# Optimization experiments

Hardware: AMD Instinct MI355X
Metric: run time of the kernel (lower is better)

Reference implementation:

```python
import jax, jax.numpy as jnp
import numpy as np

B, DIM, DIMH, DIMC = 1024, 32, 1024, 512
SQRT_HALF_PI = float(np.sqrt(np.pi / 2.0))
SQRT2 = float(np.sqrt(2.0))


def _gsp(x):
    """gaussian_softplus activation from ConditionalICNN."""
    return (SQRT_HALF_PI * x * jax.scipy.special.erf(x / SQRT2)
            + jnp.exp(-0.5 * x * x) + SQRT_HALF_PI * x) / (2.0 * SQRT_HALF_PI)


def setup_inputs() -> dict:
    key = jax.random.key(0)
    _i = [0]
    def nrm(shape, s=0.05):
        _i[0] += 1
        return jax.random.normal(jax.random.fold_in(key, _i[0]), shape, dtype=jnp.float32) * s
    inp = {
        "x": nrm((B, DIM), 1.0),
        "c": nrm((B, DIMC), 1.0),
        # w0 init: log(exp(1)-1) as in DeepConvexFlow
        "w0": jnp.full((1,), float(np.log(np.e - 1.0)), dtype=jnp.float32),
        "w1": jnp.zeros((1,), dtype=jnp.float32),
        "Wz0_w": nrm((DIMH, DIM)), "Wz0_b": nrm((DIMH,)),
        "Wc0_w": nrm((DIMH, DIMC)), "Wc0_b": nrm((DIMH,)),
        "an0_b": nrm((DIMH,)), "an0_logs": nrm((DIMH,), 0.01),
        "Wz1_w": nrm((DIMH, DIMH)), "Wz1_b": nrm((DIMH,)),
        "Wx1_w": nrm((DIMH, DIM)), "Wx1_b": nrm((DIMH,)),
        "Wc1_w": nrm((DIMH, DIMC)), "Wc1_b": nrm((DIMH,)),
        "an1_b": nrm((DIMH,)), "an1_logs": nrm((DIMH,), 0.01),
        "Wz2_w": nrm((DIMH, DIMH)), "Wz2_b": nrm((DIMH,)),
        "Wx2_w": nrm((DIMH, DIM)), "Wx2_b": nrm((DIMH,)),
        "Wc2_w": nrm((DIMH, DIMC)), "Wc2_b": nrm((DIMH,)),
        "an2_b": nrm((DIMH,)), "an2_logs": nrm((DIMH,), 0.01),
        "Wzout_w": nrm((1, DIMH)), "Wxout_w": nrm((1, DIM)), "Wcout_w": nrm((1, DIMC)),
    }
    return inp


def reference(x, c, w0, w1,
              Wz0_w, Wz0_b, Wc0_w, Wc0_b, an0_b, an0_logs,
              Wz1_w, Wz1_b, Wx1_w, Wx1_b, Wc1_w, Wc1_b, an1_b, an1_logs,
              Wz2_w, Wz2_b, Wx2_w, Wx2_b, Wc2_w, Wc2_b, an2_b, an2_logs,
              Wzout_w, Wxout_w, Wcout_w):
    """ConditionalDeepConvexFlow.forward_transform with exact logdet.
    Returns (f = grad_x F(x), logdet = logabsdet of per-sample Hessian)."""

    def pot(x1, c1):  # scalar convex potential F for one sample
        h = Wz0_w @ x1 + Wz0_b + Wc0_w @ c1 + Wc0_b
        z = _gsp((h + an0_b) * jnp.exp(an0_logs))  # ActNormNoLogdet + act
        for (Wz_w, Wz_b, Wx_w, Wx_b, Wc_w, Wc_b, an_b, an_logs) in (
                (Wz1_w, Wz1_b, Wx1_w, Wx1_b, Wc1_w, Wc1_b, an1_b, an1_logs),
                (Wz2_w, Wz2_b, Wx2_w, Wx2_b, Wc2_w, Wc2_b, an2_b, an2_logs)):
            # PosLinear: softplus(W) with gain 1/in_features
            h = (jax.nn.softplus(Wz_w) @ z) / DIMH + Wz_b \
                + Wx_w @ x1 + Wx_b + Wc_w @ c1 + Wc_b
            z = _gsp((h + an_b) * jnp.exp(an_logs))
        icnn = (jax.nn.softplus(Wzout_w) @ z)[0] / DIMH \
               + (Wxout_w @ x1)[0] + (Wcout_w @ c1)[0]
        return jax.nn.softplus(w1)[0] * icnn \
               + jax.nn.softplus(w0)[0] * 0.5 * jnp.sum(x1 * x1)

    f = jax.vmap(jax.grad(pot))(x, c)          # [B, DIM]
    H = jax.vmap(jax.hessian(pot))(x, c)       # [B, DIM, DIM]
    logdet = jnp.linalg.slogdet(H)[1]          # [B]
    return f, logdet
```

## Files before the change

kernel.cpp:

```cpp
#include <hip/hip_runtime.h>

constexpr int NB   = 1024;
constexpr int NDIM = 32;
constexpr int NH   = 1024;
constexpr int NC   = 512;
constexpr int NS   = 8;
constexpr int KSF  = 8;

constexpr float INV_SQRT2PI = 0.3989422804014327f;
constexpr float SQRT_HALF   = 0.70710678118654752f;
constexpr float SQRT_HPI    = 1.2533141373155003f;

typedef __attribute__((ext_vector_type(8))) short short8;
typedef __attribute__((ext_vector_type(4))) short short4v;
typedef __attribute__((ext_vector_type(4))) float float4v;

__device__ __forceinline__ float sp_f(float x) {
  return (x > 20.f) ? x : log1pf(expf(x));
}

__device__ __forceinline__ short f2bf(float f) {
  union { float f; unsigned u; } x; x.f = f;
  const unsigned r = x.u + 0x7fffu + ((x.u >> 16) & 1u);
  return (short)(r >> 16);
}

__device__ __forceinline__ float bf2f(short s) {
  union { unsigned u; float f; } c;
  c.u = ((unsigned)(unsigned short)s) << 16;
  return c.f;
}

__device__ __forceinline__ void async_ld16(const void* g, void* l) {
  __builtin_amdgcn_global_load_lds(
      (const __attribute__((address_space(1))) void*)g,
      (__attribute__((address_space(3))) void*)l, 16, 0, 0);
}

__global__ __launch_bounds__(256) void k_prep(
    const float* __restrict__ Wz1, const float* __restrict__ Wz2,
    const float* __restrict__ Wzout, const float* __restrict__ Wz0,
    const float* __restrict__ Wx1, const float* __restrict__ Wx2,
    const float* __restrict__ Wc0, const float* __restrict__ Wc1,
    const float* __restrict__ Wc2, const float* __restrict__ Cc,
    short* __restrict__ S1b, short* __restrict__ S1Tb,
    short* __restrict__ S2b, short* __restrict__ S2Tb,
    short* __restrict__ Wc0b, short* __restrict__ Wc1b, short* __restrict__ Wc2b,
    short* __restrict__ Ccb, short* __restrict__ W0Tb,
    short* __restrict__ Wx1Tb, short* __restrict__ Wx2Tb,
    float* __restrict__ so)
{
  const int idx = blockIdx.x * 256 + threadIdx.x;
  const int i = idx >> 10, p = idx & 1023;
  const float v1 = sp_f(Wz1[idx]);
  const short b1 = f2bf(v1);
  S1b[idx] = b1; S1Tb[p * NH + i] = b1;
  const float v2 = sp_f(Wz2[idx]);
  const short b2 = f2bf(v2);
  S2b[idx] = b2; S2Tb[p * NH + i] = b2;
  if (idx < NH) so[idx] = sp_f(Wzout[idx]);
  if (idx < NH * NC) {
    Wc0b[idx] = f2bf(Wc0[idx]);
    Wc1b[idx] = f2bf(Wc1[idx]);
    Wc2b[idx] = f2bf(Wc2[idx]);
  }
  if (idx < NB * NC) Ccb[idx] = f2bf(Cc[idx]);
  if (idx < NDIM * NH) {
    const int j = idx >> 10, pp = idx & 1023;
    W0Tb[idx]  = f2bf(Wz0[pp * NDIM + j]);
    Wx1Tb[idx] = f2bf(Wx1[pp * NDIM + j]);
    Wx2Tb[idx] = f2bf(Wx2[pp * NDIM + j]);
  }
}

__global__ __launch_bounds__(256) void k_gemmx(
    const float* __restrict__ A,
    const float* __restrict__ B0, const float* __restrict__ B1,
    const float* __restrict__ B2,
    float* __restrict__ C0, float* __restrict__ C1, float* __restrict__ C2,
    int ldc)
{
  const float* Bt = (blockIdx.z == 0) ? B0 : (blockIdx.z == 1) ? B1 : B2;
  float* C        = (blockIdx.z == 0) ? C0 : (blockIdx.z == 1) ? C1 : C2;
  __shared__ float As[16][68];
  __shared__ float Bs[16][68];
  const int tid  = threadIdx.y * 16 + threadIdx.x;
  const int arow = tid >> 2;
  const int acol = (tid & 3) << 2;
  const int m0 = blockIdx.y << 6;
  const int n0 = blockIdx.x << 6;

  float acc[4][4];
#pragma unroll
  for (int i = 0; i < 4; ++i)
#pragma unroll
    for (int j = 0; j < 4; ++j) acc[i][j] = 0.f;

  const int R = m0 + arow;
  for (int k0 = 0; k0 < NDIM; k0 += 16) {
    const float4 av = *reinterpret_cast<const float4*>(&A[(size_t)R * NDIM + k0 + acol]);
    As[acol + 0][arow] = av.x; As[acol + 1][arow] = av.y;
    As[acol + 2][arow] = av.z; As[acol + 3][arow] = av.w;
    const float4 bv = *reinterpret_cast<const float4*>(&Bt[(size_t)(n0 + arow) * NDIM + k0 + acol]);
    Bs[acol + 0][arow] = bv.x; Bs[acol + 1][arow] = bv.y;
    Bs[acol + 2][arow] = bv.z; Bs[acol + 3][arow] = bv.w;
    __syncthreads();
#pragma unroll
    for (int kk = 0; kk < 16; ++kk) {
      const float4 a  = *reinterpret_cast<const float4*>(&As[kk][threadIdx.y << 2]);
      const float4 bb = *reinterpret_cast<const float4*>(&Bs[kk][threadIdx.x << 2]);
      const float am[4] = {a.x, a.y, a.z, a.w};
      const float bn[4] = {bb.x, bb.y, bb.z, bb.w};
#pragma unroll
      for (int i2 = 0; i2 < 4; ++i2)
#pragma unroll
        for (int j2 = 0; j2 < 4; ++j2)
          acc[i2][j2] = fmaf(am[i2], bn[j2], acc[i2][j2]);
    }
    __syncthreads();
  }
#pragma unroll
  for (int i2 = 0; i2 < 4; ++i2) {
    const int row = m0 + (threadIdx.y << 2) + i2;
    const int col = n0 + (threadIdx.x << 2);
    float* cp = &C[(size_t)row * ldc + col];
    const float4 cur = *reinterpret_cast<const float4*>(cp);
    float4 o;
    o.x = acc[i2][0] + cur.x; o.y = acc[i2][1] + cur.y;
    o.z = acc[i2][2] + cur.z; o.w = acc[i2][3] + cur.w;
    *reinterpret_cast<float4*>(cp) = o;
  }
}

__global__ __launch_bounds__(256) void k_m128(
    const short* __restrict__ A, const short* __restrict__ Bt,
    float* __restrict__ C, float scale, int K, int ldc)
{
  __shared__ short As[128 * 32];
  __shared__ short Bs[128 * 32];
  const int tid  = threadIdx.x;
  const int wave = tid >> 6, lane = tid & 63;
  const int m0 = blockIdx.x << 7, n0 = blockIdx.y << 7;
  const int wm = (wave >> 1) << 6, wn = (wave & 1) << 6;
  const int qd = lane >> 4, md = lane & 15;
  const int sr = lane >> 2;
  const int sc = (lane & 3) << 3;

  float4v acc[4][4];
#pragma unroll
  for (int i = 0; i < 4; ++i)
#pragma unroll
    for (int j = 0; j < 4; ++j) acc[i][j] = (float4v)(0.f);

  for (int k0 = 0; k0 < K; k0 += 32) {
#pragma unroll
    for (int i = 0; i < 2; ++i) {
      const int ch  = wave * 2 + i;
      const int row = ch * 16 + sr;
      async_ld16(&A [(size_t)(m0 + row) * K + k0 + sc], &As[ch * 512]);
      async_ld16(&Bt[(size_t)(n0 + row) * K + k0 + sc], &Bs[ch * 512]);
    }
    __syncthreads();
    short8 af[4], bfr[4];
#pragma unroll
    for (int t = 0; t < 4; ++t) {
      af[t]  = *(const short8*)&As[(wm + t * 16 + md) * 32 + qd * 8];
      bfr[t] = *(const short8*)&Bs[(wn + t * 16 + md) * 32 + qd * 8];
    }
#pragma unroll
    for (int i = 0; i < 4; ++i)
#pragma unroll
      for (int j = 0; j < 4; ++j)
        acc[i][j] = __builtin_amdgcn_mfma_f32_16x16x32_bf16(bfr[j], af[i], acc[i][j], 0, 0, 0);
    __syncthreads();
  }

#pragma unroll
  for (int i = 0; i < 4; ++i) {
    const int rowg = m0 + wm + i * 16 + md;
#pragma unroll
    for (int j = 0; j < 4; ++j) {
      const int colb = n0 + wn + j * 16 + (qd << 2);
      float4 o;
      o.x = acc[i][j][0] * scale; o.y = acc[i][j][1] * scale;
      o.z = acc[i][j][2] * scale; o.w = acc[i][j][3] * scale;
      *reinterpret_cast<float4*>(&C[(size_t)rowg * ldc + colb]) = o;
    }
  }
}

template<int EPI>
__global__ __launch_bounds__(256) void k_mgemm(
    const short* __restrict__ A, const short* __restrict__ Bt,
    short* __restrict__ o1, short* __restrict__ o2,
    const float* __restrict__ gvec, const float* __restrict__ dvec,
    const short* __restrict__ wepiT,
    float scale, int K, int b0)
{
  __shared__ short As[128 * 32];
  __shared__ short Bs[64 * 32];
  const int tid  = threadIdx.x;
  const int wave = tid >> 6, lane = tid & 63;
  const int m0 = blockIdx.x << 7, n0 = blockIdx.y << 6;
  const int wm = (wave >> 1) << 6, wn = (wave & 1) << 5;
  const int qd = lane >> 4, md = lane & 15;
  const int sr = lane >> 2;
  const int sc = (lane & 3) << 3;

  float4v acc[4][2];
#pragma unroll
  for (int i = 0; i < 4; ++i)
#pragma unroll
    for (int j = 0; j < 2; ++j) acc[i][j] = (float4v)(0.f);

  for (int k0 = 0; k0 < K; k0 += 32) {
#pragma unroll
    for (int i = 0; i < 3; ++i) {
      const int ch = wave * 3 + i;
      if (ch < 8) {
        async_ld16(&A[(size_t)(m0 + ch * 16 + sr) * K + k0 + sc], &As[ch * 512]);
      } else {
        const int c2 = ch - 8;
        async_ld16(&Bt[(size_t)(n0 + c2 * 16 + sr) * K + k0 + sc], &Bs[c2 * 512]);
      }
    }
    __syncthreads();
    short8 af[4], bfr[2];
#pragma unroll
    for (int t = 0; t < 4; ++t)
      af[t]  = *(const short8*)&As[(wm + t * 16 + md) * 32 + qd * 8];
#pragma unroll
    for (int t = 0; t < 2; ++t)
      bfr[t] = *(const short8*)&Bs[(wn + t * 16 + md) * 32 + qd * 8];
#pragma unroll
    for (int i = 0; i < 4; ++i)
#pragma unroll
      for (int j = 0; j < 2; ++j)
        acc[i][j] = __builtin_amdgcn_mfma_f32_16x16x32_bf16(bfr[j], af[i], acc[i][j], 0, 0, 0);
    __syncthreads();
  }

  const int bbase = b0 + ((m0 + wm) >> 5);
  const size_t bNH0 = (size_t)bbase * NH, bNH1 = bNH0 + NH;
  float4 dqA[2], dqB[2], ggA[2], ggB[2];
#pragma unroll
  for (int j = 0; j < 2; ++j) {
    const int colb = n0 + wn + j * 16 + (qd << 2);
    dqA[j] = *(const float4*)&dvec[bNH0 + colb];
    dqB[j] = *(const float4*)&dvec[bNH1 + colb];
    if constexpr (EPI == 2) {
      ggA[j] = *(const float4*)&gvec[bNH0 + colb];
      ggB[j] = *(const float4*)&gvec[bNH1 + colb];
    }
  }
#pragma unroll
  for (int i = 0; i < 4; ++i) {
    const int rowg = m0 + wm + i * 16 + md;
    const int j2 = rowg & 31;
#pragma unroll
    for (int j = 0; j < 2; ++j) {
      const int colb = n0 + wn + j * 16 + (qd << 2);
      const short4v wq = *(const short4v*)&wepiT[(size_t)j2 * NH + colb];
      const float4 dq = (i < 2) ? dqA[j] : dqB[j];
      const float dqv[4] = {dq.x, dq.y, dq.z, dq.w};
      float v[4];
      short4v o1v;
#pragma unroll
      for (int r = 0; r < 4; ++r) {
        v[r] = acc[i][j][r] * scale + bf2f(wq[r]);
        o1v[r] = f2bf(v[r] * dqv[r]);
      }
      *(short4v*)&o1[(size_t)rowg * NH + colb] = o1v;
      if constexpr (EPI == 2) {
        const float4 gg = (i < 2) ? ggA[j] : ggB[j];
        const float ggv[4] = {gg.x, gg.y, gg.z, gg.w};
        short4v o2v;
#pragma unroll
        for (int r = 0; r < 4; ++r) o2v[r] = f2bf(v[r] * ggv[r]);
        *(short4v*)&o2[(size_t)rowg * NH + colb] = o2v;
      }
    }
  }
}

__global__ __launch_bounds__(256) void k_mgemm64(
    const short* __restrict__ A, const short* __restrict__ Bt,
    float* __restrict__ Cpart)
{
  __shared__ short As[64 * 32];
  __shared__ short Bs[64 * 32];
  const int tid  = threadIdx.x;
  const int wave = tid >> 6, lane = tid & 63;
  const int m0 = blockIdx.x << 6, n0 = blockIdx.y << 6;
  const int kb = blockIdx.z << 9;
  const int wm = (wave >> 1) << 5, wn = (wave & 1) << 5;
  const int qd = lane >> 4, md = lane & 15;
  const int sr = lane >> 2;
  const int sc = (lane & 3) << 3;

  float4v acc[2][2];
#pragma unroll
  for (int i = 0; i < 2; ++i)
#pragma unroll
    for (int j = 0; j < 2; ++j) acc[i][j] = (float4v)(0.f);

  for (int k0 = kb; k0 < kb + 512; k0 += 32) {
    const int row = wave * 16 + sr;
    async_ld16(&A [(size_t)(m0 + row) * NH + k0 + sc], &As[wave * 512]);
    async_ld16(&Bt[(size_t)(n0 + row) * NH + k0 + sc], &Bs[wave * 512]);
    __syncthreads();
    short8 af[2], bfr[2];
#pragma unroll
    for (int t = 0; t < 2; ++t) {
      af[t]  = *(const short8*)&As[(wm + t * 16 + md) * 32 + qd * 8];
      bfr[t] = *(const short8*)&Bs[(wn + t * 16 + md) * 32 + qd * 8];
    }
#pragma unroll
    for (int i = 0; i < 2; ++i)
#pragma unroll
      for (int j = 0; j < 2; ++j)
        acc[i][j] = __builtin_amdgcn_mfma_f32_16x16x32_bf16(bfr[j], af[i], acc[i][j], 0, 0, 0);
    __syncthreads();
  }

  float* out = Cpart + (size_t)blockIdx.z * NB * NH;
#pragma unroll
  for (int i = 0; i < 2; ++i) {
    const int rowg = m0 + wm + i * 16 + md;
#pragma unroll
    for (int j = 0; j < 2; ++j) {
      const int colb = n0 + wn + j * 16 + (qd << 2);
      float4 o;
      o.x = acc[i][j][0]; o.y = acc[i][j][1];
      o.z = acc[i][j][2]; o.w = acc[i][j][3];
      *reinterpret_cast<float4*>(&out[(size_t)rowg * NH + colb]) = o;
    }
  }
}

__global__ __launch_bounds__(256) void k_act(
    const float* __restrict__ HP2, const float* __restrict__ HPC_l,
    const float* __restrict__ bA, const float* __restrict__ bB,
    const float* __restrict__ bC,
    const float* __restrict__ anb, const float* __restrict__ anl,
    short* __restrict__ Zbf, float* __restrict__ G, float* __restrict__ U,
    int hasC, float scale)
{
  const int idx = blockIdx.x * 256 + threadIdx.x;
  const int i = idx & 1023;
  float bias = bA[i] + bB[i] + anb[i];
  if (hasC) bias += bC[i];
  const float el = expf(anl[i]);
  const float hc = HPC_l[(size_t)(idx >> 10) * (3 * NH) + i];
  const float hp = HP2 ? (HP2[idx] + HP2[(size_t)NB * NH + idx]) * scale : 0.f;
  const float a = (hp + hc + bias) * el;
  const float pdf = expf(-0.5f * a * a);
  const float er = erff(a * SQRT_HALF);
  Zbf[idx] = f2bf((SQRT_HPI * a * er + pdf + SQRT_HPI * a) * INV_SQRT2PI);
  G[idx] = 0.5f * (1.f + er) * el;
  U[idx] = pdf * INV_SQRT2PI * el * el;
}

__global__ __launch_bounds__(256) void k_act2(
    const float* __restrict__ HP2, const float* __restrict__ HPC_l,
    const float* __restrict__ bA, const float* __restrict__ bB,
    const float* __restrict__ bC,
    const float* __restrict__ anb, const float* __restrict__ anl,
    const float* __restrict__ so,
    float* __restrict__ SD2, short* __restrict__ D2gbf, float scale)
{
  const int idx = blockIdx.x * 256 + threadIdx.x;
  const int i = idx & 1023;
  const float bias = bA[i] + bB[i] + bC[i] + anb[i];
  const float el = expf(anl[i]);
  const float hc = HPC_l[(size_t)(idx >> 10) * (3 * NH) + i];
  const float hp = (HP2[idx] + HP2[(size_t)NB * NH + idx]) * scale;
  const float a = (hp + hc + bias) * el;
  const float pdf = expf(-0.5f * a * a);
  const float er = erff(a * SQRT_HALF);
  const float g = 0.5f * (1.f + er) * el;
  const float u = pdf * INV_SQRT2PI * el * el;
  const float t2 = so[i] * (1.f / NH);
  SD2[idx] = sqrtf(fmaxf(t2 * u, 0.f));
  D2gbf[idx] = f2bf(t2 * g);
}

__global__ __launch_bounds__(256) void k_bw1(
    const float* __restrict__ T2, const float* __restrict__ G1,
    const float* __restrict__ U1,
    short* __restrict__ E1bf, float* __restrict__ SD1, float scale)
{
  const int idx = blockIdx.x * 256 + threadIdx.x;
  const float t = (T2[idx] + T2[(size_t)NB * NH + idx]) * scale;
  E1bf[idx] = f2bf(t * G1[idx]);
  SD1[idx] = sqrtf(fmaxf(t * U1[idx], 0.f));
}

__global__ __launch_bounds__(256) void k_bw0(
    const float* __restrict__ T2, const float* __restrict__ U0,
    const float* __restrict__ G0,
    float* __restrict__ D0, short* __restrict__ GT0b, float scale)
{
  const int idx = blockIdx.x * 256 + threadIdx.x;
  const float t = (T2[idx] + T2[(size_t)NB * NH + idx]) * scale;
  D0[idx] = t * U0[idx];
  GT0b[idx] = f2bf(t * G0[idx]);
}

__global__ __launch_bounds__(256) void k_scale0(
    const float* __restrict__ G0, const float* __restrict__ Wz0,
    short* __restrict__ Ah1, int b0)
{
  const int idx = blockIdx.x * 256 + threadIdx.x;
  const int p = idx & 1023, r = idx >> 10;
  const int b = b0 + (r >> 5), j = r & 31;
  Ah1[idx] = f2bf(G0[(size_t)b * NH + p] * Wz0[p * NDIM + j]);
}

__global__ __launch_bounds__(256) void k_fgemm(
    const short* __restrict__ A0, const short* __restrict__ A1,
    const short* __restrict__ A2,
    const short* __restrict__ W0T, const short* __restrict__ W1T,
    const short* __restrict__ W2T,
    float* __restrict__ partF)
{
  const int mb = blockIdx.x;
  const int ks = blockIdx.y;
  const int term = blockIdx.z;
  const short* A  = (term == 0) ? A0 : (term == 1) ? A1 : A2;
  const short* WT = (term == 0) ? W0T : (term == 1) ? W1T : W2T;
  const int wave = threadIdx.x >> 6, lane = threadIdx.x & 63;
  const int qd = lane >> 4, md = lane & 15;
  const int m0 = mb * 128 + wave * 32;
  const int kbeg = ks * (NH / KSF);

  float4v acc[2][2];
#pragma unroll
  for (int i = 0; i < 2; ++i)
#pragma unroll
    for (int j = 0; j < 2; ++j) acc[i][j] = (float4v)(0.f);

  for (int k0 = kbeg; k0 < kbeg + NH / KSF; k0 += 32) {
    const int kk = k0 + qd * 8;
    short8 af[2], bfr[2];
    af[0]  = *(const short8*)&A[(size_t)(m0 + md) * NH + kk];
    af[1]  = *(const short8*)&A[(size_t)(m0 + 16 + md) * NH + kk];
    bfr[0] = *(const short8*)&WT[(size_t)md * NH + kk];
    bfr[1] = *(const short8*)&WT[(size_t)(16 + md) * NH + kk];
#pragma unroll
    for (int i = 0; i < 2; ++i)
#pragma unroll
      for (int j = 0; j < 2; ++j)
        acc[i][j] = __builtin_amdgcn_mfma_f32_16x16x32_bf16(af[i], bfr[j], acc[i][j], 0, 0, 0);
  }

  float* out = &partF[(size_t)(term * KSF + ks) * NB * 32];
#pragma unroll
  for (int i = 0; i < 2; ++i)
#pragma unroll
    for (int j = 0; j < 2; ++j)
#pragma unroll
      for (int r = 0; r < 4; ++r) {
        const int row = m0 + i * 16 + qd * 4 + r;
        const int col = j * 16 + md;
        out[(size_t)row * 32 + col] = acc[i][j][r];
      }
}

__global__ __launch_bounds__(256) void k_fred(
    const float* __restrict__ partF, const float* __restrict__ X,
    const float* __restrict__ Wxout,
    const float* __restrict__ w0p, const float* __restrict__ w1p,
    float* __restrict__ outF)
{
  const int e = blockIdx.x * 256 + threadIdx.x;
  float s = 0.f;
#pragma unroll
  for (int p = 0; p < 3 * KSF; ++p) s += partF[(size_t)p * NB * 32 + e];
  const float spw0 = sp_f(w0p[0]);
  const float spw1 = sp_f(w1p[0]);
  outF[e] = spw1 * (s + Wxout[e & 31]) + spw0 * X[e];
}

__global__ __launch_bounds__(256) void k_gram(
    const short* __restrict__ Q1, const short* __restrict__ Q2,
    const short* __restrict__ W0T, const float* __restrict__ D0,
    float* __restrict__ partH, int b0)
{
  const int ns = blockIdx.x, bl = blockIdx.y;
  const int b = b0 + bl;
  const int wave = threadIdx.x >> 6, lane = threadIdx.x & 63;
  const int wm = (wave >> 1) << 4, wn = (wave & 1) << 4;
  const int qd = lane >> 4, md = lane & 15;
  const int kbeg = ns << 7;
  const size_t rb = (size_t)bl * 32 * NH;

  float4v acc = (float4v)(0.f);

  for (int k0 = kbeg; k0 < kbeg + 128; k0 += 32) {
    const int kk = k0 + qd * 8;
    const short8 ar = *(const short8*)&W0T[(size_t)(wm + md) * NH + kk];
    float dd[8];
    *(float4*)&dd[0] = *(const float4*)&D0[(size_t)b * NH + kk];
    *(float4*)&dd[4] = *(const float4*)&D0[(size_t)b * NH + kk + 4];
    short8 af;
#pragma unroll
    for (int e = 0; e < 8; ++e) af[e] = f2bf(bf2f(ar[e]) * dd[e]);
    const short8 bfr = *(const short8*)&W0T[(size_t)(wn + md) * NH + kk];
    acc = __builtin_amdgcn_mfma_f32_16x16x32_bf16(af, bfr, acc, 0, 0, 0);
  }
#pragma unroll
  for (int l = 0; l < 2; ++l) {
    const short* Q = (l == 0) ? Q1 : Q2;
    for (int k0 = kbeg; k0 < kbeg + 128; k0 += 32) {
      const int kk = k0 + qd * 8;
      const short8 af  = *(const short8*)&Q[rb + (size_t)(wm + md) * NH + kk];
      const short8 bfr = *(const short8*)&Q[rb + (size_t)(wn + md) * NH + kk];
      acc = __builtin_amdgcn_mfma_f32_16x16x32_bf16(af, bfr, acc, 0, 0, 0);
    }
  }

  float* out = &partH[((size_t)bl * NS + ns) * 1024];
#pragma unroll
  for (int r = 0; r < 4; ++r)
    out[(wm + qd * 4 + r) * 32 + (wn + md)] = acc[r];
}

__global__ __launch_bounds__(256) void k_gram2(
    const float* __restrict__ partH,
    const float* __restrict__ w0p, const float* __restrict__ w1p,
    float* __restrict__ outLD, int b0)
{
  const int bl = blockIdx.x, b = b0 + bl, tid = threadIdx.x;
  __shared__ float sH[32][33];
  __shared__ float sred[32];
  const float spw0 = sp_f(w0p[0]);
  const float spw1 = sp_f(w1p[0]);
  const float* base = &partH[(size_t)bl * NS * 1024];
#pragma unroll
  for (int r = 0; r < 4; ++r) {
    const int e = r * 256 + tid;
    float s = 0.f;
#pragma unroll
    for (int ns = 0; ns < NS; ++ns) s += base[ns * 1024 + e];
    float h = s * spw1;
    const int row = e >> 5, col = e & 31;
    if (row == col) h += spw0;
    sH[row][col] = h;
  }
  __syncthreads();

  float ldacc = 0.f;
  for (int c = 0; c < 32; ++c) {
    if (tid >= c && tid < 32) {
      float s = sH[tid][c];
      for (int m = 0; m < c; ++m) s -= sH[tid][m] * sH[c][m];
      sred[tid] = s;
    }
    __syncthreads();
    const float sc = sred[c];
    if (tid >= c && tid < 32) {
      const float lcc = sqrtf(sc);
      sH[tid][c] = (tid == c) ? lcc : sred[tid] / lcc;
    }
    ldacc += logf(sc);
    __syncthreads();
  }
  if (tid == 0) outLD[b] = ldacc;
}

extern "C" void kernel_launch(void* const* d_in, const int* in_sizes, int n_in,
                              void* d_out, int out_size, void* d_ws, size_t ws_size,
                              hipStream_t stream)
{
  const float* X    = (const float*)d_in[0];
  const float* Cc   = (const float*)d_in[1];
  const float* w0   = (const float*)d_in[2];
  const float* w1   = (const float*)d_in[3];
  const float* Wz0w = (const float*)d_in[4];
  const float* Wz0b = (const float*)d_in[5];
  const float* Wc0w = (const float*)d_in[6];
  const float* Wc0b = (const float*)d_in[7];
  const float* an0b = (const float*)d_in[8];
  const float* an0l = (const float*)d_in[9];
  const float* Wz1w = (const float*)d_in[10];
  const float* Wz1b = (const float*)d_in[11];
  const float* Wx1w = (const float*)d_in[12];
  const float* Wx1b = (const float*)d_in[13];
  const float* Wc1w = (const float*)d_in[14];
  const float* Wc1b = (const float*)d_in[15];
  const float* an1b = (const float*)d_in[16];
  const float* an1l = (const float*)d_in[17];
  const float* Wz2w = (const float*)d_in[18];
  const float* Wz2b = (const float*)d_in[19];
  const float* Wx2w = (const float*)d_in[20];
  const float* Wx2b = (const float*)d_in[21];
  const float* Wc2w = (const float*)d_in[22];
  const float* Wc2b = (const float*)d_in[23];
  const float* an2b = (const float*)d_in[24];
  const float* an2l = (const float*)d_in[25];
  const float* Wzoutw = (const float*)d_in[26];
  const float* Wxoutw = (const float*)d_in[27];

  float* ws = (float*)d_ws;
  size_t off = 0;
  auto alloc = [&](size_t n) {
    float* p = ws + off; off += (n + 3) & ~(size_t)3; return p;
  };
  const size_t HH = (size_t)NH * NH;
  const size_t BH = (size_t)NB * NH;

  short* S1b  = (short*)alloc(HH / 2);
  short* S2b  = (short*)alloc(HH / 2);
  short* S1Tb = (short*)alloc(HH / 2);
  short* S2Tb = (short*)alloc(HH / 2);
  short* Wc0bb = (short*)alloc((size_t)NH * NC / 2);
  short* Wc1bb = (short*)alloc((size_t)NH * NC / 2);
  short* Wc2bb = (short*)alloc((size_t)NH * NC / 2);
  short* Ccb  = (short*)alloc((size_t)NB * NC / 2);
  short* W0Tb = (short*)alloc((size_t)NDIM * NH / 2);
  short* Wx1Tb = (short*)alloc((size_t)NDIM * NH / 2);
  short* Wx2Tb = (short*)alloc((size_t)NDIM * NH / 2);
  float* so   = alloc(NH);
  float* HP2  = alloc(2 * BH);
  float* HPC  = alloc((size_t)NB * 3 * NH);
  short* Z0b  = (short*)alloc(BH / 2);
  short* Z1b  = (short*)alloc(BH / 2);
  float* G0   = alloc(BH);
  float* U0   = alloc(BH);
  float* G1   = alloc(BH);
  float* U1   = alloc(BH);
  float* SD2  = alloc(BH);
  short* D2gb = (short*)alloc(BH / 2);
  short* E1b  = (short*)alloc(BH / 2);
  float* SD1  = alloc(BH);
  float* D0   = alloc(BH);
  short* GT0b = (short*)alloc(BH / 2);
  float* partF = alloc((size_t)3 * KSF * NB * 32);

  const size_t avail_f = ws_size / sizeof(float);
  int CB = 32;
  const int cands[6] = {1024, 512, 256, 128, 64, 32};
  for (int ci = 0; ci < 6; ++ci) {
    const size_t need = off + 3 * ((size_t)cands[ci] * 32 * NH / 2 + 4)
                      + (size_t)cands[ci] * NS * 1024 + 64;
    if (need <= avail_f) { CB = cands[ci]; break; }
  }
  const size_t chunk_sh = (size_t)CB * 32 * NH;
  short* Ah1 = (short*)alloc(chunk_sh / 2);
  short* A2b = (short*)alloc(chunk_sh / 2);
  short* Q1b = (short*)alloc(chunk_sh / 2);
  short* Q2b = Ah1;
  float* partH = alloc((size_t)CB * NS * 1024);

  float* outF  = (float*)d_out;
  float* outLD = (float*)d_out + NB * NDIM;

  const dim3 blk2(16, 16);
  const dim3 gridXz(16, NB / 64, 3);
  const dim3 gridE(NB * NH / 256);
  const dim3 grid64(NB / 64, NH / 64, 2);
  const dim3 gridC(NB / 128, 3 * NH / 128);
  const float invH = 1.0f / (float)NH;

  k_prep<<<dim3(HH / 256), dim3(256), 0, stream>>>(
      Wz1w, Wz2w, Wzoutw, Wz0w, Wx1w, Wx2w, Wc0w, Wc1w, Wc2w, Cc,
      S1b, S1Tb, S2b, S2Tb, Wc0bb, Wc1bb, Wc2bb, Ccb, W0Tb, Wx1Tb, Wx2Tb, so);

  k_m128<<<gridC, dim3(256), 0, stream>>>(Ccb, Wc0bb, HPC, 1.f, NC, 3 * NH);
  k_gemmx<<<gridXz, blk2, 0, stream>>>(X, Wz0w, Wx1w, Wx2w,
                                       HPC + 0 * NH, HPC + 1 * NH, HPC + 2 * NH, 3 * NH);

  k_act<<<gridE, dim3(256), 0, stream>>>(nullptr, HPC + 0 * NH, Wz0b, Wc0b, nullptr,
                                         an0b, an0l, Z0b, G0, U0, 0, 0.f);
  k_mgemm64<<<grid64, dim3(256), 0, stream>>>(Z0b, S1b, HP2);
  k_act<<<gridE, dim3(256), 0, stream>>>(HP2, HPC + 1 * NH, Wz1b, Wx1b, Wc1b,
                                         an1b, an1l, Z1b, G1, U1, 1, invH);
  k_mgemm64<<<grid64, dim3(256), 0, stream>>>(Z1b, S2b, HP2);
  k_act2<<<gridE, dim3(256), 0, stream>>>(HP2, HPC + 2 * NH, Wz2b, Wx2b, Wc2b,
                                          an2b, an2l, so, SD2, D2gb, invH);
  k_mgemm64<<<grid64, dim3(256), 0, stream>>>(D2gb, S2Tb, HP2);
  k_bw1<<<gridE, dim3(256), 0, stream>>>(HP2, G1, U1, E1b, SD1, invH);
  k_mgemm64<<<grid64, dim3(256), 0, stream>>>(E1b, S1Tb, HP2);
  k_bw0<<<gridE, dim3(256), 0, stream>>>(HP2, U0, G0, D0, GT0b, invH);

  k_fgemm<<<dim3(8, KSF, 3), dim3(256), 0, stream>>>(
      GT0b, E1b, D2gb, W0Tb, Wx1Tb, Wx2Tb, partF);
  k_fred<<<dim3(NB * 32 / 256), dim3(256), 0, stream>>>(
      partF, X, Wxoutw, w0, w1, outF);

  const dim3 gridJ(CB * 32 / 128, NH / 64);
  const dim3 gridS((size_t)CB * 32 * NH / 256);
  const dim3 gridG(NS, CB);
  for (int b0 = 0; b0 < NB; b0 += CB) {
    k_scale0<<<gridS, dim3(256), 0, stream>>>(G0, Wz0w, Ah1, b0);
    k_mgemm<2><<<gridJ, dim3(256), 0, stream>>>(Ah1, S1b, Q1b, A2b,
                                                G1, SD1, Wx1Tb, invH, NH, b0);
    k_mgemm<1><<<gridJ, dim3(256), 0, stream>>>(A2b, S2b, Q2b, nullptr,
                                                nullptr, SD2, Wx2Tb, invH, NH, b0);
    k_gram<<<gridG, dim3(256), 0, stream>>>(Q1b, Q2b, W0Tb, D0, partH, b0);
    k_gram2<<<dim3(CB), dim3(256), 0, stream>>>(partH, w0, w1, outLD, b0);
  }
}
```

Measured before the change: 721.7 us.

## Fuse activation and backward epilogues into GEMMs, drop split-K for backward GEMMs

Folds the layer-0 activation into the k_gemmx epilogue, and replaces the two split-K backward GEMMs plus their elementwise kernels (k_bw1, k_bw0) with a non-split GEMM that applies the epilogue directly. This removes kernel launches and the fp32 partial-sum round trips through memory. k_mgemm now reads its B operand straight from global memory into registers instead of staging it in LDS, and k_scale0 reads the bf16 transposed weight for coalesced access. The trade-off is half as many blocks for the backward GEMMs (no K split) and slightly different rounding from the bf16 weight.

Result: slower. 791.9 us (+9.7%).

```diff
diff --git a/kernel.cpp b/kernel.cpp
--- a/kernel.cpp
+++ b/kernel.cpp
@@ -78,7 +78,10 @@
     const float* __restrict__ B0, const float* __restrict__ B1,
     const float* __restrict__ B2,
     float* __restrict__ C0, float* __restrict__ C1, float* __restrict__ C2,
-    int ldc)
+    int ldc,
+    const float* __restrict__ bz0, const float* __restrict__ bc0,
+    const float* __restrict__ anb0, const float* __restrict__ anl0,
+    short* __restrict__ Z0b, float* __restrict__ G0, float* __restrict__ U0)
 {
   const float* Bt = (blockIdx.z == 0) ? B0 : (blockIdx.z == 1) ? B1 : B2;
   float* C        = (blockIdx.z == 0) ? C0 : (blockIdx.z == 1) ? C1 : C2;
@@ -125,10 +128,36 @@
     const int col = n0 + (threadIdx.x << 2);
     float* cp = &C[(size_t)row * ldc + col];
     const float4 cur = *reinterpret_cast<const float4*>(cp);
-    float4 o;
-    o.x = acc[i2][0] + cur.x; o.y = acc[i2][1] + cur.y;
-    o.z = acc[i2][2] + cur.z; o.w = acc[i2][3] + cur.w;
-    *reinterpret_cast<float4*>(cp) = o;
+    float o[4];
+    o[0] = acc[i2][0] + cur.x; o[1] = acc[i2][1] + cur.y;
+    o[2] = acc[i2][2] + cur.z; o[3] = acc[i2][3] + cur.w;
+    if (blockIdx.z == 0) {
+      short4v zb;
+      float4 g4, u4;
+      float gg[4], uu[4];
+#pragma unroll
+      for (int e = 0; e < 4; ++e) {
+        const int cc = col + e;
+        const float bias = bz0[cc] + bc0[cc] + anb0[cc];
+        const float el = expf(anl0[cc]);
+        const float a = (o[e] + bias) * el;
+        const float pdf = expf(-0.5f * a * a);
+        const float er = erff(a * SQRT_HALF);
+        zb[e] = f2bf((SQRT_HPI * a * er + pdf + SQRT_HPI * a) * INV_SQRT2PI);
+        gg[e] = 0.5f * (1.f + er) * el;
+        uu[e] = pdf * INV_SQRT2PI * el * el;
+      }
+      const size_t oi = (size_t)row * NH + col;
+      *(short4v*)&Z0b[oi] = zb;
+      g4.x = gg[0]; g4.y = gg[1]; g4.z = gg[2]; g4.w = gg[3];
+      u4.x = uu[0]; u4.y = uu[1]; u4.z = uu[2]; u4.w = uu[3];
+      *(float4*)&G0[oi] = g4;
+      *(float4*)&U0[oi] = u4;
+    } else {
+      float4 ov;
+      ov.x = o[0]; ov.y = o[1]; ov.z = o[2]; ov.w = o[3];
+      *reinterpret_cast<float4*>(cp) = ov;
+    }
   }
 }
 
@@ -198,7 +227,6 @@
     float scale, int K, int b0)
 {
   __shared__ short As[128 * 32];
-  __shared__ short Bs[64 * 32];
   const int tid  = threadIdx.x;
   const int wave = tid >> 6, lane = tid & 63;
   const int m0 = blockIdx.x << 7, n0 = blockIdx.y << 6;
@@ -215,23 +243,19 @@
 
   for (int k0 = 0; k0 < K; k0 += 32) {
 #pragma unroll
-    for (int i = 0; i < 3; ++i) {
-      const int ch = wave * 3 + i;
-      if (ch < 8) {
-        async_ld16(&A[(size_t)(m0 + ch * 16 + sr) * K + k0 + sc], &As[ch * 512]);
-      } else {
-        const int c2 = ch - 8;
-        async_ld16(&Bt[(size_t)(n0 + c2 * 16 + sr) * K + k0 + sc], &Bs[c2 * 512]);
-      }
-    }
-    __syncthreads();
-    short8 af[4], bfr[2];
+    for (int i = 0; i < 2; ++i) {
+      const int ch = wave * 2 + i;
+      async_ld16(&A[(size_t)(m0 + ch * 16 + sr) * K + k0 + sc], &As[ch * 512]);
+    }
+    short8 bfr[2];
+#pragma unroll
+    for (int t = 0; t < 2; ++t)
+      bfr[t] = *(const short8*)&Bt[(size_t)(n0 + wn + t * 16 + md) * K + k0 + qd * 8];
+    __syncthreads();
+    short8 af[4];
 #pragma unroll
     for (int t = 0; t < 4; ++t)
-      af[t]  = *(const short8*)&As[(wm + t * 16 + md) * 32 + qd * 8];
-#pragma unroll
-    for (int t = 0; t < 2; ++t)
-      bfr[t] = *(const short8*)&Bs[(wn + t * 16 + md) * 32 + qd * 8];
+      af[t] = *(const short8*)&As[(wm + t * 16 + md) * 32 + qd * 8];
 #pragma unroll
     for (int i = 0; i < 4; ++i)
 #pragma unroll
@@ -283,7 +307,7 @@
   }
 }
 
-__global__ __launch_bounds__(256) void k_mgemm64(
+__global__ __launch_bounds__(256) void k_mgemm64s(
     const short* __restrict__ A, const short* __restrict__ Bt,
     float* __restrict__ Cpart)
 {
@@ -338,21 +362,89 @@
   }
 }
 
+template<int FEPI>
+__global__ __launch_bounds__(256) void k_mgemm64f(
+    const short* __restrict__ A, const short* __restrict__ Bt,
+    const float* __restrict__ auxA, const float* __restrict__ auxB,
+    short* __restrict__ ob, float* __restrict__ of1,
+    float scale)
+{
+  __shared__ short As[64 * 32];
+  __shared__ short Bs[64 * 32];
+  const int tid  = threadIdx.x;
+  const int wave = tid >> 6, lane = tid & 63;
+  const int m0 = blockIdx.x << 6, n0 = blockIdx.y << 6;
+  const int wm = (wave >> 1) << 5, wn = (wave & 1) << 5;
+  const int qd = lane >> 4, md = lane & 15;
+  const int sr = lane >> 2;
+  const int sc = (lane & 3) << 3;
+
+  float4v acc[2][2];
+#pragma unroll
+  for (int i = 0; i < 2; ++i)
+#pragma unroll
+    for (int j = 0; j < 2; ++j) acc[i][j] = (float4v)(0.f);
+
+  for (int k0 = 0; k0 < NH; k0 += 32) {
+    const int row = wave * 16 + sr;
+    async_ld16(&A [(size_t)(m0 + row) * NH + k0 + sc], &As[wave * 512]);
+    async_ld16(&Bt[(size_t)(n0 + row) * NH + k0 + sc], &Bs[wave * 512]);
+    __syncthreads();
+    short8 af[2], bfr[2];
+#pragma unroll
+    for (int t = 0; t < 2; ++t) {
+      af[t]  = *(const short8*)&As[(wm + t * 16 + md) * 32 + qd * 8];
+      bfr[t] = *(const short8*)&Bs[(wn + t * 16 + md) * 32 + qd * 8];
+    }
+#pragma unroll
+    for (int i = 0; i < 2; ++i)
+#pragma unroll
+      for (int j = 0; j < 2; ++j)
+        acc[i][j] = __builtin_amdgcn_mfma_f32_16x16x32_bf16(bfr[j], af[i], acc[i][j], 0, 0, 0);
+    __syncthreads();
+  }
+
+#pragma unroll
+  for (int i = 0; i < 2; ++i) {
+    const int rowg = m0 + wm + i * 16 + md;
+#pragma unroll
+    for (int j = 0; j < 2; ++j) {
+      const int colb = n0 + wn + j * 16 + (qd << 2);
+      const size_t oi = (size_t)rowg * NH + colb;
+      const float4 g4 = *(const float4*)&auxA[oi];
+      const float4 u4 = *(const float4*)&auxB[oi];
+      const float gv[4] = {g4.x, g4.y, g4.z, g4.w};
+      const float uv[4] = {u4.x, u4.y, u4.z, u4.w};
+      short4v eb;
+      float sd[4];
+#pragma unroll
+      for (int r = 0; r < 4; ++r) {
+        const float t = acc[i][j][r] * scale;
+        eb[r] = f2bf(t * gv[r]);
+        if constexpr (FEPI == 3) sd[r] = sqrtf(fmaxf(t * uv[r], 0.f));
+        else                     sd[r] = t * uv[r];
+      }
+      *(short4v*)&ob[oi] = eb;
+      float4 s4; s4.x = sd[0]; s4.y = sd[1]; s4.z = sd[2]; s4.w = sd[3];
+      *(float4*)&of1[oi] = s4;
+    }
+  }
+}
+
 __global__ __launch_bounds__(256) void k_act(
     const float* __restrict__ HP2, const float* __restrict__ HPC_l,
     const float* __restrict__ bA, const float* __restrict__ bB,
     const float* __restrict__ bC,
     const float* __restrict__ anb, const float* __restrict__ anl,
     short* __restrict__ Zbf, float* __restrict__ G, float* __restrict__ U,
-    int hasC, float scale)
+    float scale)
 {
   const int idx = blockIdx.x * 256 + threadIdx.x;
   const int i = idx & 1023;
-  float bias = bA[i] + bB[i] + anb[i];
-  if (hasC) bias += bC[i];
+  const float bias = bA[i] + bB[i] + bC[i] + anb[i];
   const float el = expf(anl[i]);
   const float hc = HPC_l[(size_t)(idx >> 10) * (3 * NH) + i];
-  const float hp = HP2 ? (HP2[idx] + HP2[(size_t)NB * NH + idx]) * scale : 0.f;
+  const float hp = (HP2[idx] + HP2[(size_t)NB * NH + idx]) * scale;
   const float a = (hp + hc + bias) * el;
   const float pdf = expf(-0.5f * a * a);
   const float er = erff(a * SQRT_HALF);
@@ -385,36 +477,14 @@
   D2gbf[idx] = f2bf(t2 * g);
 }
 
-__global__ __launch_bounds__(256) void k_bw1(
-    const float* __restrict__ T2, const float* __restrict__ G1,
-    const float* __restrict__ U1,
-    short* __restrict__ E1bf, float* __restrict__ SD1, float scale)
-{
-  const int idx = blockIdx.x * 256 + threadIdx.x;
-  const float t = (T2[idx] + T2[(size_t)NB * NH + idx]) * scale;
-  E1bf[idx] = f2bf(t * G1[idx]);
-  SD1[idx] = sqrtf(fmaxf(t * U1[idx], 0.f));
-}
-
-__global__ __launch_bounds__(256) void k_bw0(
-    const float* __restrict__ T2, const float* __restrict__ U0,
-    const float* __restrict__ G0,
-    float* __restrict__ D0, short* __restrict__ GT0b, float scale)
-{
-  const int idx = blockIdx.x * 256 + threadIdx.x;
-  const float t = (T2[idx] + T2[(size_t)NB * NH + idx]) * scale;
-  D0[idx] = t * U0[idx];
-  GT0b[idx] = f2bf(t * G0[idx]);
-}
-
 __global__ __launch_bounds__(256) void k_scale0(
-    const float* __restrict__ G0, const float* __restrict__ Wz0,
+    const float* __restrict__ G0, const short* __restrict__ W0Tb,
     short* __restrict__ Ah1, int b0)
 {
   const int idx = blockIdx.x * 256 + threadIdx.x;
   const int p = idx & 1023, r = idx >> 10;
   const int b = b0 + (r >> 5), j = r & 31;
-  Ah1[idx] = f2bf(G0[(size_t)b * NH + p] * Wz0[p * NDIM + j]);
+  Ah1[idx] = f2bf(G0[(size_t)b * NH + p] * bf2f(W0Tb[(size_t)j * NH + p]));
 }
 
 __global__ __launch_bounds__(256) void k_fgemm(
@@ -659,7 +729,8 @@
   const dim3 blk2(16, 16);
   const dim3 gridXz(16, NB / 64, 3);
   const dim3 gridE(NB * NH / 256);
-  const dim3 grid64(NB / 64, NH / 64, 2);
+  const dim3 grid64s(NB / 64, NH / 64, 2);
+  const dim3 grid64u(NB / 64, NH / 64);
   const dim3 gridC(NB / 128, 3 * NH / 128);
   const float invH = 1.0f / (float)NH;
 
@@ -669,20 +740,17 @@
 
   k_m128<<<gridC, dim3(256), 0, stream>>>(Ccb, Wc0bb, HPC, 1.f, NC, 3 * NH);
   k_gemmx<<<gridXz, blk2, 0, stream>>>(X, Wz0w, Wx1w, Wx2w,
-                                       HPC + 0 * NH, HPC + 1 * NH, HPC + 2 * NH, 3 * NH);
-
-  k_act<<<gridE, dim3(256), 0, stream>>>(nullptr, HPC + 0 * NH, Wz0b, Wc0b, nullptr,
-                                         an0b, an0l, Z0b, G0, U0, 0, 0.f);
-  k_mgemm64<<<grid64, dim3(256), 0, stream>>>(Z0b, S1b, HP2);
+                                       HPC + 0 * NH, HPC + 1 * NH, HPC + 2 * NH, 3 * NH,
+                                       Wz0b, Wc0b, an0b, an0l, Z0b, G0, U0);
+
+  k_mgemm64s<<<grid64s, dim3(256), 0, stream>>>(Z0b, S1b, HP2);
   k_act<<<gridE, dim3(256), 0, stream>>>(HP2, HPC + 1 * NH, Wz1b, Wx1b, Wc1b,
-                                         an1b, an1l, Z1b, G1, U1, 1, invH);
-  k_mgemm64<<<grid64, dim3(256), 0, stream>>>(Z1b, S2b, HP2);
+                                         an1b, an1l, Z1b, G1, U1, invH);
+  k_mgemm64s<<<grid64s, dim3(256), 0, stream>>>(Z1b, S2b, HP2);
   k_act2<<<gridE, dim3(256), 0, stream>>>(HP2, HPC + 2 * NH, Wz2b, Wx2b, Wc2b,
                                           an2b, an2l, so, SD2, D2gb, invH);
-  k_mgemm64<<<grid64, dim3(256), 0, stream>>>(D2gb, S2Tb, HP2);
-  k_bw1<<<gridE, dim3(256), 0, stream>>>(HP2, G1, U1, E1b, SD1, invH);
-  k_mgemm64<<<grid64, dim3(256), 0, stream>>>(E1b, S1Tb, HP2);
-  k_bw0<<<gridE, dim3(256), 0, stream>>>(HP2, U0, G0, D0, GT0b, invH);
+  k_mgemm64f<3><<<grid64u, dim3(256), 0, stream>>>(D2gb, S2Tb, G1, U1, E1b, SD1, invH);
+  k_mgemm64f<4><<<grid64u, dim3(256), 0, stream>>>(E1b, S1Tb, G0, U0, GT0b, D0, invH);
 
   k_fgemm<<<dim3(8, KSF, 3), dim3(256), 0, stream>>>(
       GT0b, E1b, D2gb, W0Tb, Wx1Tb, Wx2Tb, partF);
@@ -693,7 +761,7 @@
   const dim3 gridS((size_t)CB * 32 * NH / 256);
   const dim3 gridG(NS, CB);
   for (int b0 = 0; b0 < NB; b0 += CB) {
-    k_scale0<<<gridS, dim3(256), 0, stream>>>(G0, Wz0w, Ah1, b0);
+    k_scale0<<<gridS, dim3(256), 0, stream>>>(G0, W0Tb, Ah1, b0);
     k_mgemm<2><<<gridJ, dim3(256), 0, stream>>>(Ah1, S1b, Q1b, A2b,
                                                 G1, SD1, Wx1Tb, invH, NH, b0);
     k_mgemm<1><<<gridJ, dim3(256), 0, stream>>>(A2b, S2b, Q2b, nullptr,
```
